# Kernel tuning notes

Hardware: AMD Instinct MI355X
Metric: run time of the kernel (lower is better)

## Reference

```python
import jax, jax.numpy as jnp
import numpy as np

B, S, D = 4, 2048, 1024
O = 1024
E = 8
K = 2

def setup_inputs() -> dict:
    key = jax.random.key(0)
    k1, k2, k3, k4, k5 = jax.random.split(key, 5)
    scale = 1.0 / np.sqrt(D)
    x = jax.random.normal(k1, (B, S, D), dtype=jnp.float32)
    # expert linear layers stacked: weight [E, D, O], bias [E, O]
    We = jax.random.uniform(k2, (E, D, O), dtype=jnp.float32, minval=-scale, maxval=scale)
    be = jax.random.uniform(k3, (E, O), dtype=jnp.float32, minval=-scale, maxval=scale)
    # gate linear: weight [D, E], bias [E]
    Wg = jax.random.uniform(k4, (D, E), dtype=jnp.float32, minval=-scale, maxval=scale)
    bg = jax.random.uniform(k5, (E,), dtype=jnp.float32, minval=-scale, maxval=scale)
    return {"x": x, "We": We, "be": be, "Wg": Wg, "bg": bg}

def reference(x, We, be, Wg, bg):
    b, s, d = x.shape
    x_flat = x.reshape(-1, d)                                   # [N, D]
    gates = jax.nn.softmax(x_flat @ Wg + bg, axis=-1)           # [N, E]
    topk_gates, topk_idx = jax.lax.top_k(gates, K)              # [N, K]
    topk_gates = topk_gates / jnp.sum(topk_gates, axis=1, keepdims=True)
    # dense all-expert compute (faithful to original naive MoE)
    expert_out = jnp.einsum('nd,edo->neo', x_flat, We) + be     # [N, E, O]
    # gather top-k expert outputs per token
    selected = jnp.take_along_axis(expert_out, topk_idx[:, :, None], axis=1)  # [N, K, O]
    out = jnp.sum(selected * topk_gates[:, :, None], axis=1)    # [N, O]
    return out.reshape(b, s, -1)
```

## Files before the change

### kernel.cpp

```cpp
#include <hip/hip_runtime.h>

#define N_TOK 8192
#define DDIM 1024
#define ODIM 1024
#define NEXP 8

typedef __attribute__((ext_vector_type(8))) short bf16x8;
typedef __attribute__((ext_vector_type(4))) float f32x4;

__device__ __forceinline__ unsigned int f2bf(float f) {
    unsigned int u = __float_as_uint(f);
    return (u + 0x7fffu + ((u >> 16) & 1u)) >> 16;
}
__device__ __forceinline__ float bflo(unsigned int u) { return __uint_as_float(u << 16); }
__device__ __forceinline__ float bfhi(unsigned int u) { return __uint_as_float(u & 0xffff0000u); }

__device__ __forceinline__ void async_copy16(const unsigned short* g, unsigned short* l) {
    __builtin_amdgcn_global_load_lds(
        (const __attribute__((address_space(1))) unsigned int*)g,
        (__attribute__((address_space(3))) unsigned int*)l, 16, 0, 0);
}

__global__ __launch_bounds__(256) void wet_kernel(const float* __restrict__ We,
                                                  unsigned short* __restrict__ WeT) {
    __shared__ float tile[64][65];
    const int e = blockIdx.z, d0 = blockIdx.x * 64, o0 = blockIdx.y * 64;
    const int tid = threadIdx.x;
#pragma unroll
    for (int p = 0; p < 4; ++p) {
        int idx = p * 256 + tid;
        int row = idx >> 4, c = idx & 15;
        float4 v = *(const float4*)&We[(((size_t)e * 1024 + d0 + row) << 10) + o0 + (c << 2)];
        tile[row][c * 4 + 0] = v.x; tile[row][c * 4 + 1] = v.y;
        tile[row][c * 4 + 2] = v.z; tile[row][c * 4 + 3] = v.w;
    }
    __syncthreads();
#pragma unroll
    for (int p = 0; p < 2; ++p) {
        int idx = p * 256 + tid;
        int orow = idx >> 3, c8 = idx & 7;
        unsigned int u[8];
#pragma unroll
        for (int j = 0; j < 8; ++j) u[j] = f2bf(tile[c8 * 8 + j][orow]);
        uint4 q;
        q.x = u[0] | (u[1] << 16); q.y = u[2] | (u[3] << 16);
        q.z = u[4] | (u[5] << 16); q.w = u[6] | (u[7] << 16);
        *(uint4*)&WeT[(((size_t)e * 1024 + o0 + orow) << 10) + d0 + (c8 << 3)] = q;
    }
}

__global__ __launch_bounds__(256) void gate_kernel(const float* __restrict__ x,
                                                   const float* __restrict__ Wg,
                                                   const float* __restrict__ bg,
                                                   int* __restrict__ ea, int* __restrict__ eb,
                                                   float* __restrict__ ga, float* __restrict__ gb,
                                                   unsigned short* __restrict__ xbf) {
    const int wave = threadIdx.x >> 6, lane = threadIdx.x & 63;
    const int t = blockIdx.x * 4 + wave;
    const float* xr = x + (size_t)t * DDIM;

    float4 v[4];
#pragma unroll
    for (int c = 0; c < 4; ++c) v[c] = *(const float4*)&xr[c * 256 + lane * 4];

    unsigned short* xo = xbf + (size_t)t * DDIM;
#pragma unroll
    for (int c = 0; c < 4; ++c) {
        uint2 w;
        w.x = f2bf(v[c].x) | (f2bf(v[c].y) << 16);
        w.y = f2bf(v[c].z) | (f2bf(v[c].w) << 16);
        *(uint2*)&xo[c * 256 + lane * 4] = w;
    }

    float acc[8] = {0, 0, 0, 0, 0, 0, 0, 0};
#pragma unroll
    for (int c = 0; c < 4; ++c) {
        const int dbase = c * 256 + lane * 4;
#pragma unroll
        for (int j = 0; j < 4; ++j) {
            float xv = ((const float*)&v[c])[j];
            const float4* w = (const float4*)(Wg + (size_t)(dbase + j) * 8);
            float4 w0 = w[0], w1 = w[1];
            acc[0] += xv * w0.x; acc[1] += xv * w0.y; acc[2] += xv * w0.z; acc[3] += xv * w0.w;
            acc[4] += xv * w1.x; acc[5] += xv * w1.y; acc[6] += xv * w1.z; acc[7] += xv * w1.w;
        }
    }
#pragma unroll
    for (int off = 32; off > 0; off >>= 1) {
#pragma unroll
        for (int j = 0; j < 8; ++j) acc[j] += __shfl_xor(acc[j], off, 64);
    }
    if (lane == 0) {
        float s[8];
#pragma unroll
        for (int e = 0; e < 8; ++e) s[e] = acc[e] + bg[e];
        int a = 0;
#pragma unroll
        for (int e = 1; e < 8; ++e) if (s[e] > s[a]) a = e;
        int b = (a == 0) ? 1 : 0;
#pragma unroll
        for (int e = 0; e < 8; ++e) if (e != a && e != b && s[e] > s[b]) b = e;
        float g0 = 1.0f / (1.0f + __expf(s[b] - s[a]));
        ea[t] = a; eb[t] = b; ga[t] = g0; gb[t] = 1.0f - g0;
    }
}

__global__ __launch_bounds__(256) void scatter_kernel(const int* __restrict__ ea,
                                                      const int* __restrict__ eb,
                                                      int* __restrict__ counts,
                                                      int* __restrict__ btok,
                                                      int* __restrict__ slotA,
                                                      int* __restrict__ slotB) {
    const int t = blockIdx.x * 256 + threadIdx.x;
    const int lane = threadIdx.x & 63;
#pragma unroll
    for (int pass = 0; pass < 2; ++pass) {
        const int e = (pass == 0) ? ea[t] : eb[t];
        int* slot = (pass == 0) ? slotA : slotB;
#pragma unroll
        for (int ex = 0; ex < NEXP; ++ex) {
            unsigned long long mask = __ballot(e == ex);
            if (mask) {
                int leader = __ffsll((long long)mask) - 1;
                int base = 0;
                if (lane == leader) base = atomicAdd(&counts[ex * 32], __popcll(mask));
                base = __shfl(base, leader, 64);
                if (e == ex) {
                    int pos = base + __popcll(mask & ((1ull << lane) - 1ull));
                    btok[ex * N_TOK + pos] = t;
                    slot[t] = ex * N_TOK + pos;
                }
            }
        }
    }
}

__global__ __launch_bounds__(256) void moe_gemm(const unsigned short* __restrict__ xbf,
                                                const unsigned short* __restrict__ WeT,
                                                const float* __restrict__ be,
                                                const int* __restrict__ counts,
                                                const int* __restrict__ btok,
                                                unsigned short* __restrict__ ybuf) {
    const int e = blockIdx.z;
    const int cnt = counts[e * 32];
    const int r0 = blockIdx.y * 128;
    if (r0 >= cnt) return;
    const int n0 = blockIdx.x * 128;

    __shared__ unsigned short sA[128 * 64];
    __shared__ unsigned short sB[128 * 64];
    __shared__ int s_tok[128];

    const int tid = threadIdx.x;
    if (tid < 128) {
        int r = r0 + tid;
        int rc = (r < cnt) ? r : (cnt - 1);
        s_tok[tid] = btok[e * N_TOK + rc];
    }
    const int wave = tid >> 6, lane = tid & 63;
    __syncthreads();

    const int colo = (((lane & 7) ^ (lane >> 3)) * 8);
    size_t a_off[4];
    size_t b_off[4];
#pragma unroll
    for (int p = 0; p < 4; ++p) {
        int row = wave * 32 + p * 8 + (lane >> 3);
        a_off[p] = ((size_t)s_tok[row] << 10) + colo;
        b_off[p] = (((size_t)e * 1024 + n0 + row) << 10) + colo;
    }

    const int wm = (wave >> 1) * 64, wn = (wave & 1) * 64;
    const int quad = lane >> 4, rA = lane & 15;
    const int sw = rA & 7;

    f32x4 acc[4][4];
#pragma unroll
    for (int mi = 0; mi < 4; ++mi)
#pragma unroll
        for (int ni = 0; ni < 4; ++ni) acc[mi][ni] = (f32x4){0.f, 0.f, 0.f, 0.f};

    for (int kb = 0; kb < DDIM; kb += 64) {
#pragma unroll
        for (int p = 0; p < 4; ++p) {
            unsigned short* la = &sA[(wave * 32 + p * 8) * 64];
            unsigned short* lb = &sB[(wave * 32 + p * 8) * 64];
            async_copy16(xbf + a_off[p] + kb, la);
            async_copy16(WeT + b_off[p] + kb, lb);
        }
        __syncthreads();
#pragma unroll
        for (int ks = 0; ks < 2; ++ks) {
            const int cslot = ((ks * 4 + quad) ^ sw) * 8;
            bf16x8 af[4], bfr[4];
#pragma unroll
            for (int mi = 0; mi < 4; ++mi)
                af[mi] = *(bf16x8*)&sA[(wm + mi * 16 + rA) * 64 + cslot];
#pragma unroll
            for (int ni = 0; ni < 4; ++ni)
                bfr[ni] = *(bf16x8*)&sB[(wn + ni * 16 + rA) * 64 + cslot];
#pragma unroll
            for (int mi = 0; mi < 4; ++mi)
#pragma unroll
                for (int ni = 0; ni < 4; ++ni)
                    acc[mi][ni] = __builtin_amdgcn_mfma_f32_16x16x32_bf16(af[mi], bfr[ni], acc[mi][ni], 0, 0, 0);
        }
        __syncthreads();
    }

#pragma unroll
    for (int ni = 0; ni < 4; ++ni) {
        int col = n0 + wn + ni * 16 + rA;
        float bias = be[(e << 10) + col];
#pragma unroll
        for (int mi = 0; mi < 4; ++mi) {
#pragma unroll
            for (int r = 0; r < 4; ++r) {
                int lrow = wm + mi * 16 + quad * 4 + r;
                if (r0 + lrow < cnt) {
                    ybuf[(((size_t)e * N_TOK + r0 + lrow) << 10) + col] =
                        (unsigned short)f2bf(acc[mi][ni][r] + bias);
                }
            }
        }
    }
}

__global__ __launch_bounds__(256) void combine_kernel(const unsigned short* __restrict__ ybuf,
                                                      const int* __restrict__ slotA,
                                                      const int* __restrict__ slotB,
                                                      const float* __restrict__ ga,
                                                      const float* __restrict__ gb,
                                                      float* __restrict__ out) {
    const int wave = threadIdx.x >> 6, lane = threadIdx.x & 63;
    const int t = blockIdx.x * 4 + wave;
    const unsigned short* ra = ybuf + ((size_t)slotA[t] << 10);
    const unsigned short* rb = ybuf + ((size_t)slotB[t] << 10);
    const float a = ga[t], b = gb[t];
    float* orow = out + ((size_t)t << 10);
#pragma unroll
    for (int i = 0; i < 4; ++i) {
        int c = i * 256 + lane * 4;
        uint2 ua = *(const uint2*)&ra[c];
        uint2 ub = *(const uint2*)&rb[c];
        float4 o;
        o.x = a * bflo(ua.x) + b * bflo(ub.x);
        o.y = a * bfhi(ua.x) + b * bfhi(ub.x);
        o.z = a * bflo(ua.y) + b * bflo(ub.y);
        o.w = a * bfhi(ua.y) + b * bfhi(ub.y);
        *(float4*)&orow[c] = o;
    }
}

extern "C" void kernel_launch(void* const* d_in, const int* in_sizes, int n_in,
                              void* d_out, int out_size, void* d_ws, size_t ws_size,
                              hipStream_t stream) {
    const float* x  = (const float*)d_in[0];
    const float* We = (const float*)d_in[1];
    const float* be = (const float*)d_in[2];
    const float* Wg = (const float*)d_in[3];
    const float* bg = (const float*)d_in[4];
    float* out = (float*)d_out;

    char* ws = (char*)d_ws;
    size_t off = 0;
    int* counts = (int*)(ws + off); off += 8 * 32 * 4;
    int* btok   = (int*)(ws + off); off += NEXP * N_TOK * 4;
    int* slotA  = (int*)(ws + off); off += N_TOK * 4;
    int* slotB  = (int*)(ws + off); off += N_TOK * 4;
    int* ea = (int*)(ws + off); off += N_TOK * 4;
    int* eb = (int*)(ws + off); off += N_TOK * 4;
    float* ga = (float*)(ws + off); off += N_TOK * 4;
    float* gb = (float*)(ws + off); off += N_TOK * 4;
    unsigned short* WeT  = (unsigned short*)(ws + off); off += (size_t)NEXP * DDIM * ODIM * 2;
    unsigned short* xbf  = (unsigned short*)(ws + off); off += (size_t)N_TOK * DDIM * 2;
    unsigned short* ybuf = (unsigned short*)(ws + off); off += (size_t)NEXP * N_TOK * ODIM * 2;

    hipMemsetAsync(counts, 0, 8 * 32 * sizeof(int), stream);

    wet_kernel<<<dim3(16, 16, 8), 256, 0, stream>>>(We, WeT);
    gate_kernel<<<dim3(N_TOK / 4), 256, 0, stream>>>(x, Wg, bg, ea, eb, ga, gb, xbf);
    scatter_kernel<<<dim3(N_TOK / 256), 256, 0, stream>>>(ea, eb, counts, btok, slotA, slotB);
    moe_gemm<<<dim3(ODIM / 128, N_TOK / 128, NEXP), 256, 0, stream>>>(xbf, WeT, be, counts, btok, ybuf);
    combine_kernel<<<dim3(N_TOK / 4), 256, 0, stream>>>(ybuf, slotA, slotB, ga, gb, out);
}
```

Measured before the change: 246.6 us.

## Merge weight conversion and gating into one prep kernel, reorder GEMM grid

```diff
diff --git a/kernel.cpp b/kernel.cpp
--- a/kernel.cpp
+++ b/kernel.cpp
@@ -21,97 +21,102 @@
         (__attribute__((address_space(3))) unsigned int*)l, 16, 0, 0);
 }
 
-__global__ __launch_bounds__(256) void wet_kernel(const float* __restrict__ We,
-                                                  unsigned short* __restrict__ WeT) {
-    __shared__ float tile[64][65];
-    const int e = blockIdx.z, d0 = blockIdx.x * 64, o0 = blockIdx.y * 64;
-    const int tid = threadIdx.x;
-#pragma unroll
-    for (int p = 0; p < 4; ++p) {
-        int idx = p * 256 + tid;
-        int row = idx >> 4, c = idx & 15;
-        float4 v = *(const float4*)&We[(((size_t)e * 1024 + d0 + row) << 10) + o0 + (c << 2)];
-        tile[row][c * 4 + 0] = v.x; tile[row][c * 4 + 1] = v.y;
-        tile[row][c * 4 + 2] = v.z; tile[row][c * 4 + 3] = v.w;
-    }
-    __syncthreads();
-#pragma unroll
-    for (int p = 0; p < 2; ++p) {
-        int idx = p * 256 + tid;
-        int orow = idx >> 3, c8 = idx & 7;
-        unsigned int u[8];
-#pragma unroll
-        for (int j = 0; j < 8; ++j) u[j] = f2bf(tile[c8 * 8 + j][orow]);
-        uint4 q;
-        q.x = u[0] | (u[1] << 16); q.y = u[2] | (u[3] << 16);
-        q.z = u[4] | (u[5] << 16); q.w = u[6] | (u[7] << 16);
-        *(uint4*)&WeT[(((size_t)e * 1024 + o0 + orow) << 10) + d0 + (c8 << 3)] = q;
-    }
-}
-
-__global__ __launch_bounds__(256) void gate_kernel(const float* __restrict__ x,
+__global__ __launch_bounds__(256) void prep_kernel(const float* __restrict__ x,
                                                    const float* __restrict__ Wg,
                                                    const float* __restrict__ bg,
+                                                   const float* __restrict__ We,
                                                    int* __restrict__ ea, int* __restrict__ eb,
                                                    float* __restrict__ ga, float* __restrict__ gb,
-                                                   unsigned short* __restrict__ xbf) {
-    const int wave = threadIdx.x >> 6, lane = threadIdx.x & 63;
-    const int t = blockIdx.x * 4 + wave;
-    const float* xr = x + (size_t)t * DDIM;
-
-    float4 v[4];
-#pragma unroll
-    for (int c = 0; c < 4; ++c) v[c] = *(const float4*)&xr[c * 256 + lane * 4];
-
-    unsigned short* xo = xbf + (size_t)t * DDIM;
-#pragma unroll
-    for (int c = 0; c < 4; ++c) {
-        uint2 w;
-        w.x = f2bf(v[c].x) | (f2bf(v[c].y) << 16);
-        w.y = f2bf(v[c].z) | (f2bf(v[c].w) << 16);
-        *(uint2*)&xo[c * 256 + lane * 4] = w;
-    }
-
-    float acc[8] = {0, 0, 0, 0, 0, 0, 0, 0};
-#pragma unroll
-    for (int c = 0; c < 4; ++c) {
-        const int dbase = c * 256 + lane * 4;
-#pragma unroll
-        for (int j = 0; j < 4; ++j) {
-            float xv = ((const float*)&v[c])[j];
-            const float4* w = (const float4*)(Wg + (size_t)(dbase + j) * 8);
-            float4 w0 = w[0], w1 = w[1];
-            acc[0] += xv * w0.x; acc[1] += xv * w0.y; acc[2] += xv * w0.z; acc[3] += xv * w0.w;
-            acc[4] += xv * w1.x; acc[5] += xv * w1.y; acc[6] += xv * w1.z; acc[7] += xv * w1.w;
-        }
-    }
-#pragma unroll
-    for (int off = 32; off > 0; off >>= 1) {
-#pragma unroll
-        for (int j = 0; j < 8; ++j) acc[j] += __shfl_xor(acc[j], off, 64);
-    }
-    if (lane == 0) {
-        float s[8];
-#pragma unroll
-        for (int e = 0; e < 8; ++e) s[e] = acc[e] + bg[e];
-        int a = 0;
-#pragma unroll
-        for (int e = 1; e < 8; ++e) if (s[e] > s[a]) a = e;
-        int b = (a == 0) ? 1 : 0;
-#pragma unroll
-        for (int e = 0; e < 8; ++e) if (e != a && e != b && s[e] > s[b]) b = e;
-        float g0 = 1.0f / (1.0f + __expf(s[b] - s[a]));
-        ea[t] = a; eb[t] = b; ga[t] = g0; gb[t] = 1.0f - g0;
-    }
-}
-
-__global__ __launch_bounds__(256) void scatter_kernel(const int* __restrict__ ea,
-                                                      const int* __restrict__ eb,
-                                                      int* __restrict__ counts,
-                                                      int* __restrict__ btok,
-                                                      int* __restrict__ slotA,
-                                                      int* __restrict__ slotB) {
-    const int t = blockIdx.x * 256 + threadIdx.x;
+                                                   unsigned short* __restrict__ xbf,
+                                                   unsigned short* __restrict__ WeT,
+                                                   int* __restrict__ counts) {
+    __shared__ float tile[64][65];
+    if (blockIdx.x < 2048) {
+        if (blockIdx.x == 0) counts[threadIdx.x] = 0;
+        const int wave = threadIdx.x >> 6, lane = threadIdx.x & 63;
+        const int t = blockIdx.x * 4 + wave;
+        const float* xr = x + (size_t)t * DDIM;
+
+        float4 v[4];
+#pragma unroll
+        for (int c = 0; c < 4; ++c) v[c] = *(const float4*)&xr[c * 256 + lane * 4];
+
+        unsigned short* xo = xbf + (size_t)t * DDIM;
+#pragma unroll
+        for (int c = 0; c < 4; ++c) {
+            uint2 w;
+            w.x = f2bf(v[c].x) | (f2bf(v[c].y) << 16);
+            w.y = f2bf(v[c].z) | (f2bf(v[c].w) << 16);
+            *(uint2*)&xo[c * 256 + lane * 4] = w;
+        }
+
+        float acc[8] = {0, 0, 0, 0, 0, 0, 0, 0};
+#pragma unroll
+        for (int c = 0; c < 4; ++c) {
+            const int dbase = c * 256 + lane * 4;
+#pragma unroll
+            for (int j = 0; j < 4; ++j) {
+                float xv = ((const float*)&v[c])[j];
+                const float4* w = (const float4*)(Wg + (size_t)(dbase + j) * 8);
+                float4 w0 = w[0], w1 = w[1];
+                acc[0] += xv * w0.x; acc[1] += xv * w0.y; acc[2] += xv * w0.z; acc[3] += xv * w0.w;
+                acc[4] += xv * w1.x; acc[5] += xv * w1.y; acc[6] += xv * w1.z; acc[7] += xv * w1.w;
+            }
+        }
+#pragma unroll
+        for (int off = 32; off > 0; off >>= 1) {
+#pragma unroll
+            for (int j = 0; j < 8; ++j) acc[j] += __shfl_xor(acc[j], off, 64);
+        }
+        if (lane == 0) {
+            float s[8];
+#pragma unroll
+            for (int e = 0; e < 8; ++e) s[e] = acc[e] + bg[e];
+            int a = 0;
+#pragma unroll
+            for (int e = 1; e < 8; ++e) if (s[e] > s[a]) a = e;
+            int b = (a == 0) ? 1 : 0;
+#pragma unroll
+            for (int e = 0; e < 8; ++e) if (e != a && e != b && s[e] > s[b]) b = e;
+            float g0 = 1.0f / (1.0f + __expf(s[b] - s[a]));
+            ea[t] = a; eb[t] = b; ga[t] = g0; gb[t] = 1.0f - g0;
+        }
+    } else {
+        const int lin = blockIdx.x - 2048;
+        const int e = lin >> 8, rem = lin & 255;
+        const int d0 = (rem >> 4) * 64, o0 = (rem & 15) * 64;
+        const int tid = threadIdx.x;
+#pragma unroll
+        for (int p = 0; p < 4; ++p) {
+            int idx = p * 256 + tid;
+            int row = idx >> 4, c = idx & 15;
+            float4 v = *(const float4*)&We[(((size_t)e * 1024 + d0 + row) << 10) + o0 + (c << 2)];
+            tile[row][c * 4 + 0] = v.x; tile[row][c * 4 + 1] = v.y;
+            tile[row][c * 4 + 2] = v.z; tile[row][c * 4 + 3] = v.w;
+        }
+        __syncthreads();
+#pragma unroll
+        for (int p = 0; p < 2; ++p) {
+            int idx = p * 256 + tid;
+            int orow = idx >> 3, c8 = idx & 7;
+            unsigned int u[8];
+#pragma unroll
+            for (int j = 0; j < 8; ++j) u[j] = f2bf(tile[c8 * 8 + j][orow]);
+            uint4 q;
+            q.x = u[0] | (u[1] << 16); q.y = u[2] | (u[3] << 16);
+            q.z = u[4] | (u[5] << 16); q.w = u[6] | (u[7] << 16);
+            *(uint4*)&WeT[(((size_t)e * 1024 + o0 + orow) << 10) + d0 + (c8 << 3)] = q;
+        }
+    }
+}
+
+__global__ __launch_bounds__(64) void scatter_kernel(const int* __restrict__ ea,
+                                                     const int* __restrict__ eb,
+                                                     int* __restrict__ counts,
+                                                     int* __restrict__ btok,
+                                                     int* __restrict__ slotA,
+                                                     int* __restrict__ slotB) {
+    const int t = blockIdx.x * 64 + threadIdx.x;
     const int lane = threadIdx.x & 63;
 #pragma unroll
     for (int pass = 0; pass < 2; ++pass) {
@@ -141,11 +146,12 @@
                                                 const int* __restrict__ counts,
                                                 const int* __restrict__ btok,
                                                 unsigned short* __restrict__ ybuf) {
-    const int e = blockIdx.z;
+    const int id = blockIdx.x;
+    const int e = id & 7;
+    const int n0 = ((id >> 3) & 7) * 128;
+    const int r0 = (id >> 6) * 128;
     const int cnt = counts[e * 32];
-    const int r0 = blockIdx.y * 128;
     if (r0 >= cnt) return;
-    const int n0 = blockIdx.x * 128;
 
     __shared__ unsigned short sA[128 * 64];
     __shared__ unsigned short sB[128 * 64];
@@ -239,16 +245,21 @@
     const float a = ga[t], b = gb[t];
     float* orow = out + ((size_t)t << 10);
 #pragma unroll
-    for (int i = 0; i < 4; ++i) {
-        int c = i * 256 + lane * 4;
-        uint2 ua = *(const uint2*)&ra[c];
-        uint2 ub = *(const uint2*)&rb[c];
-        float4 o;
-        o.x = a * bflo(ua.x) + b * bflo(ub.x);
-        o.y = a * bfhi(ua.x) + b * bfhi(ub.x);
-        o.z = a * bflo(ua.y) + b * bflo(ub.y);
-        o.w = a * bfhi(ua.y) + b * bfhi(ub.y);
-        *(float4*)&orow[c] = o;
+    for (int i = 0; i < 2; ++i) {
+        int c = i * 512 + lane * 8;
+        uint4 ua = *(const uint4*)&ra[c];
+        uint4 ub = *(const uint4*)&rb[c];
+        float4 o0, o1;
+        o0.x = a * bflo(ua.x) + b * bflo(ub.x);
+        o0.y = a * bfhi(ua.x) + b * bfhi(ub.x);
+        o0.z = a * bflo(ua.y) + b * bflo(ub.y);
+        o0.w = a * bfhi(ua.y) + b * bfhi(ub.y);
+        o1.x = a * bflo(ua.z) + b * bflo(ub.z);
+        o1.y = a * bfhi(ua.z) + b * bfhi(ub.z);
+        o1.z = a * bflo(ua.w) + b * bflo(ub.w);
+        o1.w = a * bfhi(ua.w) + b * bfhi(ub.w);
+        *(float4*)&orow[c] = o0;
+        *(float4*)&orow[c + 4] = o1;
     }
 }
 
@@ -276,11 +287,8 @@
     unsigned short* xbf  = (unsigned short*)(ws + off); off += (size_t)N_TOK * DDIM * 2;
     unsigned short* ybuf = (unsigned short*)(ws + off); off += (size_t)NEXP * N_TOK * ODIM * 2;
 
-    hipMemsetAsync(counts, 0, 8 * 32 * sizeof(int), stream);
-
-    wet_kernel<<<dim3(16, 16, 8), 256, 0, stream>>>(We, WeT);
-    gate_kernel<<<dim3(N_TOK / 4), 256, 0, stream>>>(x, Wg, bg, ea, eb, ga, gb, xbf);
-    scatter_kernel<<<dim3(N_TOK / 256), 256, 0, stream>>>(ea, eb, counts, btok, slotA, slotB);
-    moe_gemm<<<dim3(ODIM / 128, N_TOK / 128, NEXP), 256, 0, stream>>>(xbf, WeT, be, counts, btok, ybuf);
+    prep_kernel<<<dim3(4096), 256, 0, stream>>>(x, Wg, bg, We, ea, eb, ga, gb, xbf, WeT, counts);
+    scatter_kernel<<<dim3(N_TOK / 64), 64, 0, stream>>>(ea, eb, counts, btok, slotA, slotB);
+    moe_gemm<<<dim3(64 * 8 * 8), 256, 0, stream>>>(xbf, WeT, be, counts, btok, ybuf);
     combine_kernel<<<dim3(N_TOK / 4), 256, 0, stream>>>(ybuf, slotA, slotB, ga, gb, out);
 }
```

New measurement: 233.5 us. -5.3%, faster.
